# Kernel tuning notes

Measured on AMD Instinct MI355X. Metric: run time of the kernel, lower is better.

## Reference

```python
import jax, jax.numpy as jnp
import numpy as np

B, T, C = 64, 8192, 64  # batch, frames, phoneme classes


def setup_inputs() -> dict:
    key = jax.random.key(0)
    k1, k2 = jax.random.split(key)
    logits = jax.random.normal(k1, (B, T, C), dtype=jnp.float32)
    # realistic right-padding: per-sample lengths in [T//2, T]
    lengths = jax.random.randint(k2, (B,), T // 2, T + 1)
    padding_mask = jnp.arange(T)[None, :] >= lengths[:, None]
    return {"logits": logits, "padding_mask": padding_mask}


def reference(logits, padding_mask):
    """JoinSegmenter.logit_segment, eval path (mean-pool join).

    Faithful math: per-batch run-length encoding of argmax preds (padding -> -1),
    segment-mean of logits per run, drop runs whose value == -1, left-compact,
    zero-pad the tail and mark it in new_pad. Output is padded to T segments
    (static upper bound on the data-dependent torch output length); extra slots
    are zeros with new_pad=True, identical content-wise to the torch result.
    """
    Bb, Tt, Cc = logits.shape
    preds = jnp.argmax(logits, axis=-1)                      # [B,T]
    preds = jnp.where(padding_mask, -1, preds)

    # run-length encoding: segment id = cumsum of boundaries
    boundary = jnp.concatenate(
        [jnp.ones((Bb, 1), dtype=bool), preds[:, 1:] != preds[:, :-1]], axis=1
    )
    idx = jnp.cumsum(boundary, axis=1) - 1                   # [B,T] segment index per frame
    num_segs = idx[:, -1] + 1                                # [B]

    # segment sums / counts -> segment means (index_add + divide in torch)
    seg_sum = jax.vmap(lambda x, i: jax.ops.segment_sum(x, i, num_segments=Tt))(logits, idx)  # [B,T,C]
    counts = jax.vmap(lambda i: jax.ops.segment_sum(jnp.ones((Tt,), jnp.float32), i, num_segments=Tt))(idx)  # [B,T]
    seg_mean = seg_sum / jnp.maximum(counts, 1.0)[..., None]

    # run values u (value of pred within each run); -2 sentinel for unused slots
    b_ix = jnp.arange(Bb)[:, None]
    u = jnp.full((Bb, Tt), -2, dtype=preds.dtype).at[b_ix, idx].set(preds)

    valid = jnp.arange(Tt)[None, :] < num_segs[:, None]
    keep = (u != -1) & valid                                 # drop padding runs

    # left-compaction: scatter kept segment means to their compacted positions
    pos = jnp.cumsum(keep, axis=1) - 1
    pos = jnp.where(keep, pos, Tt)                           # out-of-bounds -> dropped
    new_logits = jnp.zeros((Bb, Tt, Cc), logits.dtype).at[b_ix, pos].set(seg_mean, mode="drop")

    new_sz = keep.sum(axis=1)                                # [B]
    new_pad = jnp.arange(Tt)[None, :] >= new_sz[:, None]
    return new_logits, new_pad
```

## Files before the change

### kernel.cpp

```cpp
#include <hip/hip_runtime.h>

#define BB 64
#define TT 8192
#define CC 64

template<int CTRL>
__device__ __forceinline__ float dppf(float x) {
    return __int_as_float(__builtin_amdgcn_update_dpp(
        0, __float_as_int(x), CTRL, 0xF, 0xF, true));
}
template<int CTRL>
__device__ __forceinline__ int dppi(int x) {
    return __builtin_amdgcn_update_dpp(0, x, CTRL, 0xF, 0xF, true);
}

__global__ __launch_bounds__(256) void k_argmax(const float* __restrict__ logits,
                                                const int* __restrict__ mask,
                                                int* __restrict__ preds) {
    const int lane = threadIdx.x & 63;
    const int wave = threadIdx.x >> 6;
    const int sub  = lane & 7;
    const int fidx = lane >> 3;
    const int wavesPerBlock = blockDim.x >> 6;
    const int gw = blockIdx.x * wavesPerBlock + wave;
    const int nw = gridDim.x * wavesPerBlock;
    const int ngroups = (BB * TT) >> 3;

    #pragma unroll 2
    for (int g = gw; g < ngroups; g += nw) {
        const int f = g * 8 + fidx;
        const float* row = logits + (size_t)f * CC + sub * 8;
        const float4 v0 = *reinterpret_cast<const float4*>(row);
        const float4 v1 = *reinterpret_cast<const float4*>(row + 4);
        float m = fmaxf(fmaxf(fmaxf(v0.x, v0.y), fmaxf(v0.z, v0.w)),
                        fmaxf(fmaxf(v1.x, v1.y), fmaxf(v1.z, v1.w)));
        m = fmaxf(m, dppf<0x141>(m));
        m = fmaxf(m, dppf<0x4E>(m));
        m = fmaxf(m, dppf<0xB1>(m));
        const int c0 = sub * 8;
        int li = 64;
        if (v1.w == m) li = c0 + 7;
        if (v1.z == m) li = c0 + 6;
        if (v1.y == m) li = c0 + 5;
        if (v1.x == m) li = c0 + 4;
        if (v0.w == m) li = c0 + 3;
        if (v0.z == m) li = c0 + 2;
        if (v0.y == m) li = c0 + 1;
        if (v0.x == m) li = c0 + 0;
        li = min(li, dppi<0x141>(li));
        li = min(li, dppi<0x4E>(li));
        li = min(li, dppi<0xB1>(li));
        if (sub == 0) preds[f] = mask[f] ? -1 : li;
    }
}

__global__ __launch_bounds__(1024) void k_rle(const int* __restrict__ preds,
                                              int* __restrict__ g_start,
                                              int* __restrict__ g_count,
                                              int* __restrict__ g_newsz) {
    __shared__ int s_pred[TT];
    __shared__ int s_start[TT];
    __shared__ int s_part[1024];
    const int b   = blockIdx.x;
    const int tid = threadIdx.x;
    const int NT  = 1024;
    const int CHUNK = TT / NT;
    const int t0 = tid * CHUNK;

    {
        const int4* src = reinterpret_cast<const int4*>(preds + (size_t)b * TT);
        int4* dst = reinterpret_cast<int4*>(s_pred);
        for (int i = tid; i < TT / 4; i += NT) dst[i] = src[i];
    }
    __syncthreads();

    int local = 0;
    for (int t = t0; t < t0 + CHUNK; ++t) {
        int bnd = (t == 0) || (s_pred[t] != s_pred[t - 1]);
        local += bnd;
    }
    s_part[tid] = local;
    __syncthreads();
    for (int off = 1; off < NT; off <<= 1) {
        int v = (tid >= off) ? s_part[tid - off] : 0;
        __syncthreads();
        s_part[tid] += v;
        __syncthreads();
    }
    const int num_segs = s_part[NT - 1];
    int run = (tid > 0) ? s_part[tid - 1] : 0;
    for (int t = t0; t < t0 + CHUNK; ++t) {
        int bnd = (t == 0) || (s_pred[t] != s_pred[t - 1]);
        if (bnd) { run++; s_start[run - 1] = t; }
    }
    __syncthreads();

    int lk = 0;
    for (int s = t0; s < t0 + CHUNK; ++s) {
        if (s < num_segs && s_pred[s_start[s]] != -1) lk++;
    }
    __syncthreads();
    s_part[tid] = lk;
    __syncthreads();
    for (int off = 1; off < NT; off <<= 1) {
        int v = (tid >= off) ? s_part[tid - off] : 0;
        __syncthreads();
        s_part[tid] += v;
        __syncthreads();
    }
    int pos = (tid > 0) ? s_part[tid - 1] : 0;
    for (int s = t0; s < t0 + CHUNK; ++s) {
        if (s < num_segs) {
            const int st = s_start[s];
            if (s_pred[st] != -1) {
                const int end = (s + 1 < num_segs) ? s_start[s + 1] : TT;
                g_start[(size_t)b * TT + pos] = st;
                g_count[(size_t)b * TT + pos] = end - st;
                pos++;
            }
        }
    }
    if (tid == 0) g_newsz[b] = s_part[NT - 1];
}

__global__ __launch_bounds__(256) void k_out(const float* __restrict__ logits,
                                             const int* __restrict__ g_start,
                                             const int* __restrict__ g_count,
                                             const int* __restrict__ g_newsz,
                                             float* __restrict__ out_logits,
                                             float* __restrict__ out_pad) {
    __shared__ int s_nsz[BB];
    if (threadIdx.x < BB) s_nsz[threadIdx.x] = g_newsz[threadIdx.x];
    __syncthreads();

    const int lane = threadIdx.x & 63;
    const int wave = threadIdx.x >> 6;
    const int sub  = lane & 15;
    const int ridx = lane >> 4;
    const int wavesPerBlock = blockDim.x >> 6;
    const int gw = blockIdx.x * wavesPerBlock + wave;
    const int nw = gridDim.x * wavesPerBlock;
    const int ngroups = (BB * TT) >> 2;

    for (int g = gw; g < ngroups; g += nw) {
        const int row = g * 4 + ridx;
        const int b = row >> 13;
        const int p = row & (TT - 1);
        const int nsz = s_nsz[b];
        float4 val = make_float4(0.f, 0.f, 0.f, 0.f);
        if (p < nsz) {
            const int st  = g_start[row];
            const int cnt = g_count[row];
            const float* src = logits + ((size_t)b * TT + st) * CC + sub * 4;
            float4 acc = *reinterpret_cast<const float4*>(src);
            for (int f = 1; f < cnt; ++f) {
                const float4 v = *reinterpret_cast<const float4*>(src + (size_t)f * CC);
                acc.x += v.x; acc.y += v.y; acc.z += v.z; acc.w += v.w;
            }
            const float inv = 1.0f / (float)cnt;
            val = make_float4(acc.x * inv, acc.y * inv, acc.z * inv, acc.w * inv);
        }
        *reinterpret_cast<float4*>(out_logits + (size_t)row * CC + sub * 4) = val;
        if (sub == 0) out_pad[row] = (p >= nsz) ? 1.0f : 0.0f;
    }
}

extern "C" void kernel_launch(void* const* d_in, const int* in_sizes, int n_in,
                              void* d_out, int out_size, void* d_ws, size_t ws_size,
                              hipStream_t stream) {
    const float* logits = (const float*)d_in[0];
    const int*   mask   = (const int*)d_in[1];

    int* preds   = (int*)d_ws;
    int* g_start = preds   + (size_t)BB * TT;
    int* g_count = g_start + (size_t)BB * TT;
    int* g_newsz = g_count + (size_t)BB * TT;

    float* out_logits = (float*)d_out;
    float* out_pad    = out_logits + (size_t)BB * TT * CC;

    hipLaunchKernelGGL(k_argmax, dim3(2048), dim3(256), 0, stream,
                       logits, mask, preds);
    hipLaunchKernelGGL(k_rle, dim3(BB), dim3(1024), 0, stream,
                       preds, g_start, g_count, g_newsz);
    hipLaunchKernelGGL(k_out, dim3(2048), dim3(256), 0, stream,
                       logits, g_start, g_count, g_newsz, out_logits, out_pad);
}
```

Measured before the change: 79.32 us.

## Move pad writes into RLE kernel, widen output rows, use nontemporal stores

The padding-mask output is now written by the RLE kernel with vectorized nontemporal stores, so the output kernel no longer does it with scattered scalar writes. The output kernel switches to 8 lanes per row, each handling two float4s, and writes results with nontemporal stores to bypass the cache. The argmax loop unroll goes from 2 to 4. Fewer, wider lanes per row mean more rows in flight per wave but fewer lanes per gather, and the RLE kernel takes on a small amount of extra store work.

Measured after the change: 91.65 us. 1.16x slower.

```diff
diff --git a/kernel.cpp b/kernel.cpp
--- a/kernel.cpp
+++ b/kernel.cpp
@@ -3,6 +3,8 @@
 #define BB 64
 #define TT 8192
 #define CC 64
+
+typedef float vfloat4 __attribute__((ext_vector_type(4)));
 
 template<int CTRL>
 __device__ __forceinline__ float dppf(float x) {
@@ -26,7 +28,7 @@
     const int nw = gridDim.x * wavesPerBlock;
     const int ngroups = (BB * TT) >> 3;
 
-    #pragma unroll 2
+    #pragma unroll 4
     for (int g = gw; g < ngroups; g += nw) {
         const int f = g * 8 + fidx;
         const float* row = logits + (size_t)f * CC + sub * 8;
@@ -57,7 +59,8 @@
 __global__ __launch_bounds__(1024) void k_rle(const int* __restrict__ preds,
                                               int* __restrict__ g_start,
                                               int* __restrict__ g_count,
-                                              int* __restrict__ g_newsz) {
+                                              int* __restrict__ g_newsz,
+                                              float* __restrict__ out_pad) {
     __shared__ int s_pred[TT];
     __shared__ int s_start[TT];
     __shared__ int s_part[1024];
@@ -120,48 +123,62 @@
             }
         }
     }
-    if (tid == 0) g_newsz[b] = s_part[NT - 1];
+    const int nsz = s_part[NT - 1];
+    if (tid == 0) g_newsz[b] = nsz;
+
+    float* padrow = out_pad + (size_t)b * TT;
+    for (int i = tid; i < TT / 4; i += NT) {
+        const int p = i * 4;
+        vfloat4 v = { p     >= nsz ? 1.f : 0.f,
+                      p + 1 >= nsz ? 1.f : 0.f,
+                      p + 2 >= nsz ? 1.f : 0.f,
+                      p + 3 >= nsz ? 1.f : 0.f };
+        __builtin_nontemporal_store(v, reinterpret_cast<vfloat4*>(padrow + p));
+    }
 }
 
 __global__ __launch_bounds__(256) void k_out(const float* __restrict__ logits,
                                              const int* __restrict__ g_start,
                                              const int* __restrict__ g_count,
                                              const int* __restrict__ g_newsz,
-                                             float* __restrict__ out_logits,
-                                             float* __restrict__ out_pad) {
+                                             float* __restrict__ out_logits) {
     __shared__ int s_nsz[BB];
     if (threadIdx.x < BB) s_nsz[threadIdx.x] = g_newsz[threadIdx.x];
     __syncthreads();
 
     const int lane = threadIdx.x & 63;
     const int wave = threadIdx.x >> 6;
-    const int sub  = lane & 15;
-    const int ridx = lane >> 4;
+    const int sub  = lane & 7;
+    const int ridx = lane >> 3;
     const int wavesPerBlock = blockDim.x >> 6;
     const int gw = blockIdx.x * wavesPerBlock + wave;
     const int nw = gridDim.x * wavesPerBlock;
-    const int ngroups = (BB * TT) >> 2;
+    const int ngroups = (BB * TT) >> 3;
 
     for (int g = gw; g < ngroups; g += nw) {
-        const int row = g * 4 + ridx;
+        const int row = g * 8 + ridx;
         const int b = row >> 13;
         const int p = row & (TT - 1);
         const int nsz = s_nsz[b];
-        float4 val = make_float4(0.f, 0.f, 0.f, 0.f);
+        vfloat4 o0 = {0.f, 0.f, 0.f, 0.f};
+        vfloat4 o1 = {0.f, 0.f, 0.f, 0.f};
         if (p < nsz) {
             const int st  = g_start[row];
             const int cnt = g_count[row];
-            const float* src = logits + ((size_t)b * TT + st) * CC + sub * 4;
-            float4 acc = *reinterpret_cast<const float4*>(src);
+            const float* src = logits + ((size_t)b * TT + st) * CC + sub * 8;
+            vfloat4 a0 = *reinterpret_cast<const vfloat4*>(src);
+            vfloat4 a1 = *reinterpret_cast<const vfloat4*>(src + 4);
             for (int f = 1; f < cnt; ++f) {
-                const float4 v = *reinterpret_cast<const float4*>(src + (size_t)f * CC);
-                acc.x += v.x; acc.y += v.y; acc.z += v.z; acc.w += v.w;
+                a0 += *reinterpret_cast<const vfloat4*>(src + (size_t)f * CC);
+                a1 += *reinterpret_cast<const vfloat4*>(src + (size_t)f * CC + 4);
             }
             const float inv = 1.0f / (float)cnt;
-            val = make_float4(acc.x * inv, acc.y * inv, acc.z * inv, acc.w * inv);
+            o0 = a0 * inv;
+            o1 = a1 * inv;
         }
-        *reinterpret_cast<float4*>(out_logits + (size_t)row * CC + sub * 4) = val;
-        if (sub == 0) out_pad[row] = (p >= nsz) ? 1.0f : 0.0f;
+        float* dst = out_logits + (size_t)row * CC + sub * 8;
+        __builtin_nontemporal_store(o0, reinterpret_cast<vfloat4*>(dst));
+        __builtin_nontemporal_store(o1, reinterpret_cast<vfloat4*>(dst + 4));
     }
 }
 
@@ -182,7 +199,7 @@
     hipLaunchKernelGGL(k_argmax, dim3(2048), dim3(256), 0, stream,
                        logits, mask, preds);
     hipLaunchKernelGGL(k_rle, dim3(BB), dim3(1024), 0, stream,
-                       preds, g_start, g_count, g_newsz);
+                       preds, g_start, g_count, g_newsz, out_pad);
     hipLaunchKernelGGL(k_out, dim3(2048), dim3(256), 0, stream,
-                       logits, g_start, g_count, g_newsz, out_logits, out_pad);
-}
+                       logits, g_start, g_count, g_newsz, out_logits);
+}
```
